# Kernel tuning notes

Measured on AMD Instinct MI355X. Metric: run time of the kernel, lower is better.

## Reference

```python
import jax, jax.numpy as jnp
import numpy as np

N = 128        # grid size per dimension
H = 1.0        # grid spacing (module init arg h)
NITER = 128    # Jacobi iterations: enough for wavefront to cross the grid
BIG = 1.0e5    # 'infinity' padding value for boundary neighbors
U0_FAR = 1.0e3 # initial value away from source


def _local_solve(ax, ay, az, fh):
    """Upwind local eikonal solver at each cell.
    ax, ay, az: min of the two axis neighbors per cell. fh = f * h.
    """
    a = jnp.sort(jnp.stack([ax, ay, az], axis=0), axis=0)
    a1, a2, a3 = a[0], a[1], a[2]
    # 1D update
    x1 = a1 + fh
    # 2D update: solve (x-a1)^2 + (x-a2)^2 = fh^2
    disc2 = 2.0 * fh * fh - (a1 - a2) ** 2
    x2 = 0.5 * (a1 + a2 + jnp.sqrt(jnp.maximum(disc2, 0.0)))
    # 3D update: solve sum_i (x-ai)^2 = fh^2
    s = a1 + a2 + a3
    q = a1 * a1 + a2 * a2 + a3 * a3
    disc3 = s * s - 3.0 * (q - fh * fh)
    x3 = (s + jnp.sqrt(jnp.maximum(disc3, 0.0))) / 3.0
    return jnp.where(x1 <= a2, x1, jnp.where(x2 <= a3, x2, x3))


def _step(u, fh):
    up = jnp.pad(u, 1, constant_values=BIG)
    ax = jnp.minimum(up[:-2, 1:-1, 1:-1], up[2:, 1:-1, 1:-1])
    ay = jnp.minimum(up[1:-1, :-2, 1:-1], up[1:-1, 2:, 1:-1])
    az = jnp.minimum(up[1:-1, 1:-1, :-2], up[1:-1, 1:-1, 2:])
    x = _local_solve(ax, ay, az, fh)
    return jnp.minimum(u, x)  # monotone Gauss-Seidel/Jacobi update


def _solve(u0, f):
    fh = f * jnp.float32(H)

    def body(u, _):
        return _step(u, fh), None

    u, _ = jax.lax.scan(jax.checkpoint(body), u0, None, length=NITER)
    return u


def setup_inputs() -> dict:
    key = jax.random.key(0)
    kf = jax.random.fold_in(key, 1)
    # slowness field in [0.5, 1.5]
    f = 0.5 + jax.random.uniform(kf, (N, N, N), dtype=jnp.float32)
    # initial travel-time: large everywhere, 0 at source (grid center)
    u0 = jnp.full((N, N, N), U0_FAR, dtype=jnp.float32)
    u0 = u0.at[N // 2, N // 2, N // 2].set(0.0)
    return {"u0": u0, "f": f}


def reference(u0, f):
    return _solve(u0, f)
```

## Files before the change

kernel.cpp:

```cpp
#include <hip/hip_runtime.h>

#define GN    128
#define GBIG  1.0e5f
#define NITER 128

#define PPY     130
#define PITCH_Y 128
#define PITCH_Z (128 * 130)
#define PADDED_TOTAL (130 * 130 * 128)

__global__ __launch_bounds__(256) void eik_init(const float* __restrict__ u0,
                                                const float* __restrict__ f,
                                                float* __restrict__ uA,
                                                float* __restrict__ uB,
                                                float* __restrict__ fP) {
    const int i = blockIdx.x * 256 + threadIdx.x;
    if (i >= PADDED_TOTAL) return;
    const int x = i & 127;
    const int r = i >> 7;
    const int y = r % 130;
    const int z = r / 130;
    float uv = GBIG, fv = 0.0f;
    if (y >= 1 && y <= GN && z >= 1 && z <= GN) {
        const int src = ((z - 1) * GN + (y - 1)) * GN + x;
        uv = u0[src];
        fv = f[src];
    }
    uA[i] = uv;
    uB[i] = uv;
    fP[i] = fv;
}

__device__ __forceinline__ float eik_solve(float ax, float ay, float az,
                                           float fh, float uc) {
    const float a1 = fminf(fminf(ax, ay), az);
    const float a3 = fmaxf(fmaxf(ax, ay), az);
    const float a2 = fmaxf(fminf(fmaxf(ax, ay), az), fminf(ax, ay));
    const float x1 = a1 + fh;
    const float d12 = a1 - a2;
    const float disc2 = 2.0f * fh * fh - d12 * d12;
    const float x2 = 0.5f * (a1 + a2 + sqrtf(fmaxf(disc2, 0.0f)));
    const float s = a1 + a2 + a3;
    const float q = a1 * a1 + a2 * a2 + a3 * a3;
    const float disc3 = s * s - 3.0f * (q - fh * fh);
    const float x3 = (s + sqrtf(fmaxf(disc3, 0.0f))) * (1.0f / 3.0f);
    const float xv = (x1 <= a2) ? x1 : ((x2 <= a3) ? x2 : x3);
    return fminf(uc, xv);
}

__global__ __launch_bounds__(256) void eik_step(const float* __restrict__ uin,
                                                const float* __restrict__ fP,
                                                float* __restrict__ uout,
                                                int iter) {
    const int lx = threadIdx.x;
    const int gy = blockIdx.y * 8 + threadIdx.y;
    const int gz = blockIdx.z;

    const int x0 = 4 * lx;
    const int dxm = (x0 <= 64 && 64 <= x0 + 3)
                        ? 0
                        : min(abs(x0 - 64), abs(x0 + 3 - 64));
    const int d = dxm + abs(gy - 64) + abs(gz - 64);
    if (d > iter) return;

    const int y = gy + 1;
    const int z = gz + 1;
    const int base = (z * PPY + y) * PITCH_Y + x0;

    const float4 c  = *(const float4*)(uin + base);
    float xm_s = uin[base - 1];
    float xp_s = uin[base + 4];
    if (lx == 0)  xm_s = GBIG;
    if (lx == 31) xp_s = GBIG;
    const float4 ym = *(const float4*)(uin + base - PITCH_Y);
    const float4 yp = *(const float4*)(uin + base + PITCH_Y);
    const float4 zm = *(const float4*)(uin + base - PITCH_Z);
    const float4 zp = *(const float4*)(uin + base + PITCH_Z);
    const float4 f4 = *(const float4*)(fP + base);

    float4 res;
    res.x = eik_solve(fminf(xm_s, c.y), fminf(ym.x, yp.x), fminf(zm.x, zp.x),
                      f4.x, c.x);
    res.y = eik_solve(fminf(c.x, c.z), fminf(ym.y, yp.y), fminf(zm.y, zp.y),
                      f4.y, c.y);
    res.z = eik_solve(fminf(c.y, c.w), fminf(ym.z, yp.z), fminf(zm.z, zp.z),
                      f4.z, c.z);
    res.w = eik_solve(fminf(c.z, xp_s), fminf(ym.w, yp.w), fminf(zm.w, zp.w),
                      f4.w, c.w);

    *(float4*)(uout + base) = res;
}

__global__ __launch_bounds__(256) void eik_extract(const float* __restrict__ uf,
                                                   float* __restrict__ out) {
    const int j = blockIdx.x * 256 + threadIdx.x;
    const int x4 = j & 31;
    const int y  = (j >> 5) & 127;
    const int z  = j >> 12;
    const float4 v =
        *(const float4*)(uf + ((z + 1) * PPY + (y + 1)) * PITCH_Y + 4 * x4);
    *(float4*)(out + 4 * j) = v;
}

extern "C" void kernel_launch(void* const* d_in, const int* in_sizes, int n_in,
                              void* d_out, int out_size, void* d_ws, size_t ws_size,
                              hipStream_t stream) {
    const float* u0 = (const float*)d_in[0];
    const float* f  = (const float*)d_in[1];
    float* out = (float*)d_out;

    float* uA = (float*)d_ws;
    float* uB = uA + PADDED_TOTAL;
    float* fP = uB + PADDED_TOTAL;

    {
        const int nb = (PADDED_TOTAL + 255) / 256;
        eik_init<<<nb, 256, 0, stream>>>(u0, f, uA, uB, fP);
    }

    const dim3 block(32, 8, 1);
    const dim3 grid(1, 16, 128);
    for (int i = 1; i <= NITER; ++i) {
        const float* in = (i & 1) ? uA : uB;
        float* o        = (i & 1) ? uB : uA;
        eik_step<<<grid, block, 0, stream>>>(in, fP, o, i);
    }

    eik_extract<<<GN * GN * GN / 4 / 256, 256, 0, stream>>>(uA, out);
}
```

Baseline: 728.1 us.

## Replace per-iteration launches with persistent cooperative kernel using neighbor flag sync

Swaps 128 separate stencil launches for one persistent cooperative kernel. Each block owns a 2-z-slab tile, keeps its cells and slowness in registers, and waits only on per-block progress flags of its four y/z neighbors through cache-bypassing polling, not a grid barrier. The aim is to remove launch overhead and global syncs and to fold the output extraction into the kernel. In exchange it relies on all 1024 blocks being co-resident, and correctness depends on hand-written inline-asm coherence loads and stores.

```diff
diff --git a/kernel.cpp b/kernel.cpp
--- a/kernel.cpp
+++ b/kernel.cpp
@@ -9,12 +9,20 @@
 #define PITCH_Z (128 * 130)
 #define PADDED_TOTAL (130 * 130 * 128)
 
+#define NBY  16
+#define NBZ  64
+#define NBLK (NBY * NBZ)
+
+typedef float fx4 __attribute__((ext_vector_type(4)));
+
 __global__ __launch_bounds__(256) void eik_init(const float* __restrict__ u0,
                                                 const float* __restrict__ f,
                                                 float* __restrict__ uA,
                                                 float* __restrict__ uB,
-                                                float* __restrict__ fP) {
+                                                float* __restrict__ fP,
+                                                int* __restrict__ flags) {
     const int i = blockIdx.x * 256 + threadIdx.x;
+    if (i < NBLK) flags[i] = 0;
     if (i >= PADDED_TOTAL) return;
     const int x = i & 127;
     const int r = i >> 7;
@@ -48,6 +56,140 @@
     return fminf(uc, xv);
 }
 
+__global__ __launch_bounds__(256, 4) void eik_persist(float* __restrict__ uA,
+                                                      float* __restrict__ uB,
+                                                      const float* __restrict__ fP,
+                                                      float* __restrict__ out,
+                                                      int* __restrict__ flags) {
+    const int lx = threadIdx.x;
+    const int ty = threadIdx.y;
+    const int by = blockIdx.y;
+    const int bz = blockIdx.z;
+    const int tid = ty * 32 + lx;
+    const int gy  = by * 8 + ty;
+    const int gz0 = bz * 2;
+    const int x0  = lx * 4;
+
+    const int dxm = (x0 <= 64 && 64 <= x0 + 3) ? 0
+                                               : min(abs(x0 - 64), abs(x0 + 3 - 64));
+    const int dy = abs(gy - 64);
+    const int d0 = dxm + dy + abs(gz0 - 64);
+    const int d1 = dxm + dy + abs(gz0 + 1 - 64);
+
+    const int ry0 = by * 8, ry1 = ry0 + 7;
+    const int dymin = (ry0 > 64) ? (ry0 - 64) : ((ry1 < 64) ? (64 - ry1) : 0);
+    const int dzmin = (gz0 > 64) ? (gz0 - 64) : ((gz0 + 1 < 64) ? (64 - (gz0 + 1)) : 0);
+    const int start = max(1, dymin + dzmin);
+
+    const int idx = bz * NBY + by;
+    if (tid == 0 && start > 1)
+        __hip_atomic_store(&flags[idx], start - 1, __ATOMIC_RELAXED,
+                           __HIP_MEMORY_SCOPE_AGENT);
+
+    const int base0 = ((gz0 + 1) * PPY + (gy + 1)) * PITCH_Y + x0;
+    const int base1 = base0 + PITCH_Z;
+    const int vo0  = base0 * 4;
+    const int vo1  = base1 * 4;
+    const int vozm = vo0 - PITCH_Z * 4;
+    const int vozp = vo1 + PITCH_Z * 4;
+
+    const int own = idx * 4;
+    const int fo0 = (by > 0)       ? own - 4       : own;
+    const int fo1 = (by < NBY - 1) ? own + 4       : own;
+    const int fo2 = (bz > 0)       ? own - 4 * NBY : own;
+    const int fo3 = (bz < NBZ - 1) ? own + 4 * NBY : own;
+
+    fx4 c0 = *(const fx4*)(uA + base0);
+    fx4 c1 = *(const fx4*)(uA + base1);
+    const fx4 f0 = *(const fx4*)(fP + base0);
+    const fx4 f1 = *(const fx4*)(fP + base1);
+
+    int s0 = 0, s1 = 0, s2 = 0, s3 = 0;
+
+    for (int i = start; i <= NITER; ++i) {
+        const int target = i - 1;
+
+        if (tid < 64) {
+            int m = min(min(s0, s1), min(s2, s3));
+            while (m < target) {
+                asm volatile(
+                    "global_load_dword %0, %4, %8 sc0 sc1\n\t"
+                    "global_load_dword %1, %5, %8 sc0 sc1\n\t"
+                    "global_load_dword %2, %6, %8 sc0 sc1\n\t"
+                    "global_load_dword %3, %7, %8 sc0 sc1\n\t"
+                    "s_waitcnt vmcnt(0)"
+                    : "=&v"(s0), "=&v"(s1), "=&v"(s2), "=&v"(s3)
+                    : "v"(fo0), "v"(fo1), "v"(fo2), "v"(fo3), "s"(flags)
+                    : "memory");
+                m = min(min(s0, s1), min(s2, s3));
+                if (m < target) {
+                    if (target - m > 2) __builtin_amdgcn_s_sleep(32);
+                    else                __builtin_amdgcn_s_sleep(1);
+                }
+            }
+        }
+        __syncthreads();
+
+        const float* S = (i & 1) ? uA : uB;
+        fx4 ym0, yp0, ym1, yp1, zm, zp;
+        asm volatile(
+            "global_load_dwordx4 %0, %6, %10 offset:-512 sc0 sc1\n\t"
+            "global_load_dwordx4 %1, %6, %10 offset:512 sc0 sc1\n\t"
+            "global_load_dwordx4 %2, %7, %10 offset:-512 sc0 sc1\n\t"
+            "global_load_dwordx4 %3, %7, %10 offset:512 sc0 sc1\n\t"
+            "global_load_dwordx4 %4, %8, %10 sc0 sc1\n\t"
+            "global_load_dwordx4 %5, %9, %10 sc0 sc1\n\t"
+            "s_waitcnt vmcnt(0)"
+            : "=&v"(ym0), "=&v"(yp0), "=&v"(ym1), "=&v"(yp1), "=&v"(zm), "=&v"(zp)
+            : "v"(vo0), "v"(vo1), "v"(vozm), "v"(vozp), "s"(S)
+            : "memory");
+
+        float xm0 = __shfl_up(c0.w, 1);   if (lx == 0)  xm0 = GBIG;
+        float xp0 = __shfl_down(c0.x, 1); if (lx == 31) xp0 = GBIG;
+        float xm1 = __shfl_up(c1.w, 1);   if (lx == 0)  xm1 = GBIG;
+        float xp1 = __shfl_down(c1.x, 1); if (lx == 31) xp1 = GBIG;
+
+        fx4 n0, n1;
+        n0.x = eik_solve(fminf(xm0,  c0.y), fminf(ym0.x, yp0.x), fminf(zm.x, c1.x), f0.x, c0.x);
+        n0.y = eik_solve(fminf(c0.x, c0.z), fminf(ym0.y, yp0.y), fminf(zm.y, c1.y), f0.y, c0.y);
+        n0.z = eik_solve(fminf(c0.y, c0.w), fminf(ym0.z, yp0.z), fminf(zm.z, c1.z), f0.z, c0.z);
+        n0.w = eik_solve(fminf(c0.z, xp0),  fminf(ym0.w, yp0.w), fminf(zm.w, c1.w), f0.w, c0.w);
+        n1.x = eik_solve(fminf(xm1,  c1.y), fminf(ym1.x, yp1.x), fminf(c0.x, zp.x), f1.x, c1.x);
+        n1.y = eik_solve(fminf(c1.x, c1.z), fminf(ym1.y, yp1.y), fminf(c0.y, zp.y), f1.y, c1.y);
+        n1.z = eik_solve(fminf(c1.y, c1.w), fminf(ym1.z, yp1.z), fminf(c0.z, zp.z), f1.z, c1.z);
+        n1.w = eik_solve(fminf(c1.z, xp1),  fminf(ym1.w, yp1.w), fminf(c0.w, zp.w), f1.w, c1.w);
+
+        const bool act0 = (d0 <= i);
+        const bool act1 = (d1 <= i);
+
+        if (i < NITER) {
+            float* D = (i & 1) ? uB : uA;
+            if (act0) {
+                c0 = n0;
+                asm volatile("global_store_dwordx4 %0, %1, %2 sc0 sc1"
+                             :: "v"(vo0), "v"(c0), "s"(D) : "memory");
+            }
+            if (act1) {
+                c1 = n1;
+                asm volatile("global_store_dwordx4 %0, %1, %2 sc0 sc1"
+                             :: "v"(vo1), "v"(c1), "s"(D) : "memory");
+            }
+            asm volatile("s_waitcnt vmcnt(0)" ::: "memory");
+            __syncthreads();
+            if (tid == 0)
+                __hip_atomic_store(&flags[idx], i, __ATOMIC_RELAXED,
+                                   __HIP_MEMORY_SCOPE_AGENT);
+        } else {
+            if (act0) c0 = n0;
+            if (act1) c1 = n1;
+        }
+    }
+
+    float* o = out + (gz0 * GN + gy) * GN + x0;
+    *(fx4*)o = c0;
+    *(fx4*)(o + GN * GN) = c1;
+}
+
 __global__ __launch_bounds__(256) void eik_step(const float* __restrict__ uin,
                                                 const float* __restrict__ fP,
                                                 float* __restrict__ uout,
@@ -55,7 +197,6 @@
     const int lx = threadIdx.x;
     const int gy = blockIdx.y * 8 + threadIdx.y;
     const int gz = blockIdx.z;
-
     const int x0 = 4 * lx;
     const int dxm = (x0 <= 64 && 64 <= x0 + 3)
                         ? 0
@@ -79,14 +220,10 @@
     const float4 f4 = *(const float4*)(fP + base);
 
     float4 res;
-    res.x = eik_solve(fminf(xm_s, c.y), fminf(ym.x, yp.x), fminf(zm.x, zp.x),
-                      f4.x, c.x);
-    res.y = eik_solve(fminf(c.x, c.z), fminf(ym.y, yp.y), fminf(zm.y, zp.y),
-                      f4.y, c.y);
-    res.z = eik_solve(fminf(c.y, c.w), fminf(ym.z, yp.z), fminf(zm.z, zp.z),
-                      f4.z, c.z);
-    res.w = eik_solve(fminf(c.z, xp_s), fminf(ym.w, yp.w), fminf(zm.w, zp.w),
-                      f4.w, c.w);
+    res.x = eik_solve(fminf(xm_s, c.y), fminf(ym.x, yp.x), fminf(zm.x, zp.x), f4.x, c.x);
+    res.y = eik_solve(fminf(c.x, c.z), fminf(ym.y, yp.y), fminf(zm.y, zp.y), f4.y, c.y);
+    res.z = eik_solve(fminf(c.y, c.w), fminf(ym.z, yp.z), fminf(zm.z, zp.z), f4.z, c.z);
+    res.w = eik_solve(fminf(c.z, xp_s), fminf(ym.w, yp.w), fminf(zm.w, zp.w), f4.w, c.w);
 
     *(float4*)(uout + base) = res;
 }
@@ -112,10 +249,27 @@
     float* uA = (float*)d_ws;
     float* uB = uA + PADDED_TOTAL;
     float* fP = uB + PADDED_TOTAL;
+    int* flags = (int*)(fP + PADDED_TOTAL);
 
     {
         const int nb = (PADDED_TOTAL + 255) / 256;
-        eik_init<<<nb, 256, 0, stream>>>(u0, f, uA, uB, fP);
+        eik_init<<<nb, 256, 0, stream>>>(u0, f, uA, uB, fP, flags);
+    }
+
+    static int coop_ok = -1;
+    if (coop_ok < 0) {
+        int maxb = 0;
+        hipError_t qe =
+            hipOccupancyMaxActiveBlocksPerMultiprocessor(&maxb, eik_persist, 256, 0);
+        coop_ok = (qe == hipSuccess && maxb >= 4) ? 1 : 0;
+    }
+
+    if (coop_ok) {
+        void* args[] = {(void*)&uA, (void*)&uB, (void*)&fP, (void*)&out, (void*)&flags};
+        hipError_t e = hipLaunchCooperativeKernel((void*)eik_persist,
+                                                  dim3(1, NBY, NBZ), dim3(32, 8, 1),
+                                                  args, 0, stream);
+        if (e == hipSuccess) return;
     }
 
     const dim3 block(32, 8, 1);
@@ -125,6 +279,5 @@
         float* o        = (i & 1) ? uB : uA;
         eik_step<<<grid, block, 0, stream>>>(in, fP, o, i);
     }
-
     eik_extract<<<GN * GN * GN / 4 / 256, 256, 0, stream>>>(uA, out);
 }
```

Result: no change. 729.1 us (+0.1%).
